# Performance work log

Measured on AMD Instinct MI355X. Metric: run time of the kernel, lower is better.

## Reference

```python
import jax, jax.numpy as jnp
import numpy as np

H, D = 16, 64            # heads_num, mouse_hidden_dim // heads_num
START_FRAME = 9728       # current_start (token units)
GLOBAL_END_PREV = 9728   # kv_cache['global_end_index'] before this call
LOCAL_END_PREV = 9728    # kv_cache['local_end_index'] before this call
SINK = 0                 # sink_tokens in source
WINDOW = 8192            # max_attention_size = local_attn_size (token units)


def _rope_interleaved(x, cos_h, sin_h):
    # non-neox (interleaved) rotary: x [B,S,H,D], cos_h/sin_h [S, D//2]
    x1 = x[..., 0::2]
    x2 = x[..., 1::2]
    c = cos_h[None, :, None, :]
    s = sin_h[None, :, None, :]
    o1 = x1 * c - x2 * s
    o2 = x2 * c + x1 * s
    return jnp.stack([o1, o2], axis=-1).reshape(x.shape)


def setup_inputs() -> dict:
    key = jax.random.key(0)
    ks = jax.random.split(key, 7)
    B, S, C = 1, 1024, 10240
    return {
        'q': jax.random.normal(ks[0], (B, S, H, D), jnp.float32),
        'k': jax.random.normal(ks[1], (B, S, H, D), jnp.float32),
        'v': jax.random.normal(ks[2], (B, S, H, D), jnp.float32),
        'cache_k': jax.random.normal(ks[3], (B, C, H, D), jnp.float32),
        'cache_v': jax.random.normal(ks[4], (B, C, H, D), jnp.float32),
        'freqs_cos': jax.random.uniform(ks[5], (START_FRAME + S, D), jnp.float32, -1.0, 1.0),
        'freqs_sin': jax.random.uniform(ks[6], (START_FRAME + S, D), jnp.float32, -1.0, 1.0),
    }


def reference(q, k, v, cache_k, cache_v, freqs_cos, freqs_sin):
    B, S, _, _ = q.shape
    # _apply_rotary_emb_qk: slice freqs at start_offset, take every-other col (cos_half)
    cos_h = freqs_cos[START_FRAME:START_FRAME + S, ::2]  # [S, D//2]
    sin_h = freqs_sin[START_FRAME:START_FRAME + S, ::2]
    q_r = _rope_interleaved(q, cos_h, sin_h)
    k_r = _rope_interleaved(k, cos_h, sin_h)

    # ring-buffer KV-cache update (all index math is static Python ints)
    current_end = START_FRAME + S
    cache_size = cache_k.shape[1]
    num_new = S
    if current_end > GLOBAL_END_PREV and num_new + LOCAL_END_PREV > cache_size:
        num_evicted = num_new + LOCAL_END_PREV - cache_size
        num_rolled = LOCAL_END_PREV - num_evicted - SINK
        rolled_k = jax.lax.dynamic_slice_in_dim(cache_k, SINK + num_evicted, num_rolled, axis=1)
        rolled_v = jax.lax.dynamic_slice_in_dim(cache_v, SINK + num_evicted, num_rolled, axis=1)
        cache_k = cache_k.at[:, SINK:SINK + num_rolled].set(rolled_k)
        cache_v = cache_v.at[:, SINK:SINK + num_rolled].set(rolled_v)
        local_end = LOCAL_END_PREV + current_end - GLOBAL_END_PREV - num_evicted
    else:
        local_end = LOCAL_END_PREV + current_end - GLOBAL_END_PREV
    local_start = local_end - num_new
    cache_k = cache_k.at[:, local_start:local_end].set(k_r)
    cache_v = cache_v.at[:, local_start:local_end].set(v)

    # windowed (last local_attn_size tokens) non-causal attention
    cache_start = max(0, local_end - WINDOW)
    wk = cache_k[:, cache_start:local_end]  # [B, W, H, D]
    wv = cache_v[:, cache_start:local_end]
    scale = 1.0 / np.float32(np.sqrt(D))
    scores = jnp.einsum('bqhd,bkhd->bhqk', q_r, wk) * scale
    probs = jax.nn.softmax(scores, axis=-1)
    out = jnp.einsum('bhqk,bkhd->bqhd', probs, wv)
    return out.reshape(B, S, H * D)
```

## Files before the change

kernel.cpp:

```cpp
#include <hip/hip_runtime.h>

#define HH 16
#define DD 64
#define SQ 1024
#define LW 8192
#define OLDK 7168
#define CACHE_BASE 2560
#define SFRAME 9728
#define KSPLIT 8
#define KPER (LW / KSPLIT)
#define NSTEP (KPER / 64)

#define KB_OFF 0u
#define VT_OFF 16777216u
#define QB_OFF 33554432u
#define OP_OFF 35651584u
#define LP_OFF 69206016u

typedef __bf16 bf16x8 __attribute__((ext_vector_type(8)));
typedef float floatx16 __attribute__((ext_vector_type(16)));
typedef float floatx2 __attribute__((ext_vector_type(2)));
typedef unsigned uintx2 __attribute__((ext_vector_type(2)));
typedef unsigned uintx4 __attribute__((ext_vector_type(4)));

__device__ __forceinline__ unsigned short f2bf(float f) {
  unsigned u = __builtin_bit_cast(unsigned, f);
  u += 0x7fffu + ((u >> 16) & 1u);
  return (unsigned short)(u >> 16);
}

__device__ __forceinline__ float fast_exp2(float x) {
#if __has_builtin(__builtin_amdgcn_exp2f)
  return __builtin_amdgcn_exp2f(x);
#else
  return __builtin_exp2f(x);
#endif
}

__device__ __forceinline__ unsigned pack_bf2(float a, float b) {
#if __has_builtin(__builtin_amdgcn_cvt_pk_bf16_f32)
  typedef __bf16 bf16x2_t __attribute__((ext_vector_type(2)));
  bf16x2_t r = __builtin_amdgcn_cvt_pk_bf16_f32(a, b);
  return __builtin_bit_cast(unsigned, r);
#else
  unsigned ua = __builtin_bit_cast(unsigned, a) + 0x8000u;
  unsigned ub = __builtin_bit_cast(unsigned, b) + 0x8000u;
  return __builtin_amdgcn_perm(ub, ua, 0x07060302);
#endif
}

__device__ __forceinline__ void async16(void* lds, const void* g) {
  __builtin_amdgcn_global_load_lds((__attribute__((address_space(1))) void*)(g),
                                   (__attribute__((address_space(3))) void*)(lds),
                                   16, 0, 0);
}

__global__ __launch_bounds__(256) void prepass(
    const float* __restrict__ qin, const float* __restrict__ kin,
    const float* __restrict__ vin, const float* __restrict__ ck,
    const float* __restrict__ cv, const float* __restrict__ fc,
    const float* __restrict__ fs, unsigned short* __restrict__ Kb,
    unsigned short* __restrict__ Vt, unsigned short* __restrict__ Qb) {
  __shared__ unsigned short tl[128 * 66];
  int b = blockIdx.x, t = threadIdx.x;
  if (b < 1024) {
    int h = b >> 6, kk0 = (b & 63) * 128;
    int c = t & 15;
#pragma unroll
    for (int it = 0; it < 8; it++) {
      int kk = it * 16 + (t >> 4);
      int gk = kk0 + kk;
      const float* src = (gk < OLDK)
                             ? cv + (CACHE_BASE + gk) * (HH * DD) + h * DD + 4 * c
                             : vin + (gk - OLDK) * (HH * DD) + h * DD + 4 * c;
      float4 vv = *(const float4*)src;
      ushort2 p0, p1;
      p0.x = f2bf(vv.x); p0.y = f2bf(vv.y);
      p1.x = f2bf(vv.z); p1.y = f2bf(vv.w);
      *(ushort2*)(tl + kk * 66 + 4 * c) = p0;
      *(ushort2*)(tl + kk * 66 + 4 * c + 2) = p1;
    }
    __syncthreads();
    int kq = t & 15;
#pragma unroll
    for (int jt = 0; jt < 4; jt++) {
      int d = jt * 16 + (t >> 4);
      ushort4 lo, hi;
      unsigned short tmp[8];
#pragma unroll
      for (int j = 0; j < 8; j++) {
        int kk = 8 * kq + j;
        tmp[j] = tl[kk * 66 + d];
      }
      lo.x = tmp[0]; lo.y = tmp[1]; lo.z = tmp[2]; lo.w = tmp[3];
      hi.x = tmp[4]; hi.y = tmp[5]; hi.z = tmp[6]; hi.w = tmp[7];
      unsigned short* dst = Vt + (h * DD + d) * LW + kk0 + 8 * kq;
      *(ushort4*)(dst) = lo;
      *(ushort4*)(dst + 4) = hi;
    }
  } else if (b < 8192) {
    int b1 = b - 1024;
    int h = b1 / 448, g = b1 % 448;
    int kk = g * 16 + (t >> 4);
    int lane = t & 15;
    float4 val = *(const float4*)(ck + (CACHE_BASE + kk) * (HH * DD) + h * DD + lane * 4);
    ushort4 o;
    o.x = f2bf(val.x); o.y = f2bf(val.y); o.z = f2bf(val.z); o.w = f2bf(val.w);
    *(ushort4*)(Kb + (h * LW + kk) * DD + lane * 4) = o;
  } else if (b < 10240) {
    int b2 = b - 8192;
    int rh = b2 * 8 + (t >> 5);
    int s = rh >> 4, h = rh & 15, i = t & 31;
    float2 x = *(const float2*)(kin + s * (HH * DD) + h * DD + 2 * i);
    float c = fc[(SFRAME + s) * DD + 2 * i];
    float sn = fs[(SFRAME + s) * DD + 2 * i];
    ushort2 o;
    o.x = f2bf(x.x * c - x.y * sn);
    o.y = f2bf(x.y * c + x.x * sn);
    *(ushort2*)(Kb + (h * LW + OLDK + s) * DD + 2 * i) = o;
  } else {
    int b3 = b - 10240;
    int rh = b3 * 8 + (t >> 5);
    int s = rh >> 4, h = rh & 15, i = t & 31;
    const float SC = 0.18033688011112042f;
    float2 x = *(const float2*)(qin + s * (HH * DD) + h * DD + 2 * i);
    float c = fc[(SFRAME + s) * DD + 2 * i];
    float sn = fs[(SFRAME + s) * DD + 2 * i];
    ushort2 o;
    o.x = f2bf((x.x * c - x.y * sn) * SC);
    o.y = f2bf((x.y * c + x.x * sn) * SC);
    *(ushort2*)(Qb + (h * SQ + s) * DD + 2 * i) = o;
  }
}

__global__ __launch_bounds__(256, 2) void attn(
    const unsigned short* __restrict__ Kb, const unsigned short* __restrict__ Vt,
    const unsigned short* __restrict__ Qb, unsigned short* __restrict__ Op,
    float* __restrict__ Lp) {
  __shared__ __align__(16) unsigned char sK[2][8192];
  __shared__ __align__(16) unsigned char sV[2][8192];

  int bid = blockIdx.x;
  int g = bid & 127, qb = bid >> 7;
  int h = g & 15, ks = g >> 4;
  int t = threadIdx.x;
  int w = t >> 6, lane = t & 63;
  int l31 = lane & 31, e = lane >> 5;
  int q0 = qb * 256 + w * 64;

  int baseA = (l31 & 7) ^ ((l31 >> 3) & 7);
  int baseB = (l31 & 7) ^ (((l31 >> 3) + 4) & 7);

  bf16x8 qf[2][4];
#pragma unroll
  for (int tq = 0; tq < 2; tq++) {
    const unsigned short* qptr = Qb + (h * SQ + q0 + 32 * tq + l31) * DD + 8 * e;
#pragma unroll
    for (int c = 0; c < 4; c++) qf[tq][c] = *(const bf16x8*)(qptr + 16 * c);
  }

  floatx16 o[2][2];
#pragma unroll
  for (int a = 0; a < 2; a++)
#pragma unroll
    for (int bb = 0; bb < 2; bb++)
#pragma unroll
      for (int i = 0; i < 16; i++) o[a][bb][i] = 0.f;
  float ls[2] = {0.f, 0.f};

  const floatx16 fz = {0.f};

  const unsigned short* KbH = Kb + h * (LW * DD);
  const unsigned short* VtH = Vt + h * (DD * LW);
  int kkBase = ks * KPER;

  int gi0 = w * 128 + lane;
  int gi1 = gi0 + 64;
  int rr0 = gi0 >> 3, rr1 = gi1 >> 3;
  int sw0 = (gi0 & 7) ^ (rr0 & 7) ^ ((rr0 >> 3) & 7);
  int sw1 = (gi1 & 7) ^ (rr1 & 7) ^ ((rr1 >> 3) & 7);
  const unsigned short* gK0 = KbH + (kkBase + rr0) * DD + sw0 * 8;
  const unsigned short* gK1 = KbH + (kkBase + rr1) * DD + sw1 * 8;
  const unsigned short* gV0 = VtH + rr0 * LW + kkBase + sw0 * 8;
  const unsigned short* gV1 = VtH + rr1 * LW + kkBase + sw1 * 8;
  int d0 = gi0 * 16, d1 = gi1 * 16;

  auto stage = [&](unsigned char* bK, unsigned char* bV) {
    async16(bK + d0, gK0);
    async16(bV + d0, gV0);
    async16(bK + d1, gK1);
    async16(bV + d1, gV1);
    gK0 += 64 * DD; gK1 += 64 * DD;
    gV0 += 64;      gV1 += 64;
  };

  auto softmax_half = [&](floatx16& sv, int tq, int tk, bf16x8 pf[2][4]) {
#pragma unroll
    for (int i = 0; i < 16; i++) sv[i] = fast_exp2(sv[i]);
    floatx2 t0, t1, t2, t3;
    t0[0] = sv[0];  t0[1] = sv[1];
    t1[0] = sv[2];  t1[1] = sv[3];
    t2[0] = sv[4];  t2[1] = sv[5];
    t3[0] = sv[6];  t3[1] = sv[7];
    floatx2 u0 = t0 + t1, u1 = t2 + t3;
    floatx2 t4, t5, t6, t7;
    t4[0] = sv[8];  t4[1] = sv[9];
    t5[0] = sv[10]; t5[1] = sv[11];
    t6[0] = sv[12]; t6[1] = sv[13];
    t7[0] = sv[14]; t7[1] = sv[15];
    floatx2 u2 = t4 + t5, u3 = t6 + t7;
    floatx2 v0 = u0 + u1, v1 = u2 + u3;
    floatx2 vs = v0 + v1;
    ls[tq] += vs[0] + vs[1];
#pragma unroll
    for (int kcp = 0; kcp < 2; kcp++) {
      unsigned u0p = pack_bf2(sv[8 * kcp + 0], sv[8 * kcp + 1]);
      unsigned u1p = pack_bf2(sv[8 * kcp + 2], sv[8 * kcp + 3]);
      unsigned u2p = pack_bf2(sv[8 * kcp + 4], sv[8 * kcp + 5]);
      unsigned u3p = pack_bf2(sv[8 * kcp + 6], sv[8 * kcp + 7]);
      uintx2 r0 = __builtin_amdgcn_permlane32_swap(u0p, u2p, false, false);
      uintx2 r1 = __builtin_amdgcn_permlane32_swap(u1p, u3p, false, false);
      uintx4 f;
      f[0] = r0[0]; f[1] = r1[0]; f[2] = r0[1]; f[3] = r1[1];
      pf[tq][2 * tk + kcp] = __builtin_bit_cast(bf16x8, f);
    }
  };

  auto step = [&](const unsigned char* cK, const unsigned char* cV,
                  bool doStage, unsigned char* nK, unsigned char* nV) {
    bf16x8 pf[2][4];

    floatx16 sA0, sA1;
    {
      int p0 = e ^ baseA;
      bf16x8 ka0 = *(const bf16x8*)(cK + (l31 * 8 + p0) * 16);
      sA0 = __builtin_amdgcn_mfma_f32_32x32x16_bf16(ka0, qf[0][0], fz, 0, 0, 0);
      sA1 = __builtin_amdgcn_mfma_f32_32x32x16_bf16(ka0, qf[1][0], fz, 0, 0, 0);
#pragma unroll
      for (int c = 1; c < 4; c++) {
        int p = (2 * c + e) ^ baseA;
        bf16x8 ka = *(const bf16x8*)(cK + (l31 * 8 + p) * 16);
        sA0 = __builtin_amdgcn_mfma_f32_32x32x16_bf16(ka, qf[0][c], sA0, 0, 0, 0);
        sA1 = __builtin_amdgcn_mfma_f32_32x32x16_bf16(ka, qf[1][c], sA1, 0, 0, 0);
      }
    }

    if (doStage) stage(nK, nV);

    floatx16 sB0, sB1;
    {
      int p0 = e ^ baseB;
      bf16x8 kb0 = *(const bf16x8*)(cK + ((l31 + 32) * 8 + p0) * 16);
      sB0 = __builtin_amdgcn_mfma_f32_32x32x16_bf16(kb0, qf[0][0], fz, 0, 0, 0);
      sB1 = __builtin_amdgcn_mfma_f32_32x32x16_bf16(kb0, qf[1][0], fz, 0, 0, 0);
#pragma unroll
      for (int c = 1; c < 4; c++) {
        int p = (2 * c + e) ^ baseB;
        bf16x8 kb = *(const bf16x8*)(cK + ((l31 + 32) * 8 + p) * 16);
        sB0 = __builtin_amdgcn_mfma_f32_32x32x16_bf16(kb, qf[0][c], sB0, 0, 0, 0);
        sB1 = __builtin_amdgcn_mfma_f32_32x32x16_bf16(kb, qf[1][c], sB1, 0, 0, 0);
      }
    }

    softmax_half(sA0, 0, 0, pf);
    softmax_half(sA1, 1, 0, pf);

#pragma unroll
    for (int kc = 0; kc < 2; kc++) {
      int pA = (2 * kc + e) ^ baseA;
      int pB = (2 * kc + e) ^ baseB;
      bf16x8 va = *(const bf16x8*)(cV + (l31 * 8 + pA) * 16);
      bf16x8 vb = *(const bf16x8*)(cV + ((l31 + 32) * 8 + pB) * 16);
      o[0][0] = __builtin_amdgcn_mfma_f32_32x32x16_bf16(va, pf[0][kc], o[0][0], 0, 0, 0);
      o[0][1] = __builtin_amdgcn_mfma_f32_32x32x16_bf16(vb, pf[0][kc], o[0][1], 0, 0, 0);
      o[1][0] = __builtin_amdgcn_mfma_f32_32x32x16_bf16(va, pf[1][kc], o[1][0], 0, 0, 0);
      o[1][1] = __builtin_amdgcn_mfma_f32_32x32x16_bf16(vb, pf[1][kc], o[1][1], 0, 0, 0);
    }

    softmax_half(sB0, 0, 1, pf);
    softmax_half(sB1, 1, 1, pf);

#pragma unroll
    for (int kc = 2; kc < 4; kc++) {
      int pA = (2 * kc + e) ^ baseA;
      int pB = (2 * kc + e) ^ baseB;
      bf16x8 va = *(const bf16x8*)(cV + (l31 * 8 + pA) * 16);
      bf16x8 vb = *(const bf16x8*)(cV + ((l31 + 32) * 8 + pB) * 16);
      o[0][0] = __builtin_amdgcn_mfma_f32_32x32x16_bf16(va, pf[0][kc], o[0][0], 0, 0, 0);
      o[0][1] = __builtin_amdgcn_mfma_f32_32x32x16_bf16(vb, pf[0][kc], o[0][1], 0, 0, 0);
      o[1][0] = __builtin_amdgcn_mfma_f32_32x32x16_bf16(va, pf[1][kc], o[1][0], 0, 0, 0);
      o[1][1] = __builtin_amdgcn_mfma_f32_32x32x16_bf16(vb, pf[1][kc], o[1][1], 0, 0, 0);
    }
  };

  stage(sK[0], sV[0]);

  for (int st = 0; st < NSTEP; st += 2) {
    __syncthreads();
    step(sK[0], sV[0], true, sK[1], sV[1]);
    __syncthreads();
    step(sK[1], sV[1], st + 2 < NSTEP, sK[0], sV[0]);
  }

#pragma unroll
  for (int tq = 0; tq < 2; tq++) {
    float l = ls[tq];
    l += __shfl_xor(l, 32, 64);
    int qrow = q0 + 32 * tq + l31;
    unsigned short* op = Op + (((ks * 16 + h) * SQ) + qrow) * DD;
#pragma unroll
    for (int t4 = 0; t4 < 4; t4++) {
      uint2 a, b;
      a.x = pack_bf2(o[tq][0][4 * t4 + 0], o[tq][0][4 * t4 + 1]);
      a.y = pack_bf2(o[tq][0][4 * t4 + 2], o[tq][0][4 * t4 + 3]);
      b.x = pack_bf2(o[tq][1][4 * t4 + 0], o[tq][1][4 * t4 + 1]);
      b.y = pack_bf2(o[tq][1][4 * t4 + 2], o[tq][1][4 * t4 + 3]);
      *(uint2*)(op + 8 * t4 + 4 * e) = a;
      *(uint2*)(op + 32 + 8 * t4 + 4 * e) = b;
    }
    if (e == 0) Lp[(ks * 16 + h) * SQ + qrow] = l;
  }
}

__global__ __launch_bounds__(256) void combine(const unsigned short* __restrict__ Op,
                                               const float* __restrict__ Lp,
                                               float* __restrict__ out) {
  int idx = blockIdx.x * 256 + threadIdx.x;
  int d4 = idx & 15, q = (idx >> 4) & 1023, h = idx >> 14;
  float num[4] = {0.f, 0.f, 0.f, 0.f};
  float den = 0.f;
#pragma unroll
  for (int s = 0; s < KSPLIT; s++) {
    int row = (s * 16 + h) * SQ + q;
    uint2 pkv = *(const uint2*)(Op + row * DD + 4 * d4);
    num[0] += __builtin_bit_cast(float, pkv.x << 16);
    num[1] += __builtin_bit_cast(float, pkv.x & 0xffff0000u);
    num[2] += __builtin_bit_cast(float, pkv.y << 16);
    num[3] += __builtin_bit_cast(float, pkv.y & 0xffff0000u);
    den += Lp[row];
  }
  float r = 1.0f / den;
  float4 ov;
  ov.x = num[0] * r; ov.y = num[1] * r; ov.z = num[2] * r; ov.w = num[3] * r;
  *(float4*)(out + q * (HH * DD) + h * DD + 4 * d4) = ov;
}

extern "C" void kernel_launch(void* const* d_in, const int* in_sizes, int n_in,
                              void* d_out, int out_size, void* d_ws, size_t ws_size,
                              hipStream_t stream) {
  const float* q  = (const float*)d_in[0];
  const float* k  = (const float*)d_in[1];
  const float* v  = (const float*)d_in[2];
  const float* ck = (const float*)d_in[3];
  const float* cv = (const float*)d_in[4];
  const float* fc = (const float*)d_in[5];
  const float* fs = (const float*)d_in[6];
  float* out = (float*)d_out;
  char* ws = (char*)d_ws;

  unsigned short* Kb = (unsigned short*)(ws + KB_OFF);
  unsigned short* Vt = (unsigned short*)(ws + VT_OFF);
  unsigned short* Qb = (unsigned short*)(ws + QB_OFF);
  unsigned short* Op = (unsigned short*)(ws + OP_OFF);
  float* Lp = (float*)(ws + LP_OFF);

  prepass<<<12288, 256, 0, stream>>>(q, k, v, ck, cv, fc, fs, Kb, Vt, Qb);
  attn<<<512, 256, 0, stream>>>(Kb, Vt, Qb, Op, Lp);
  combine<<<1024, 256, 0, stream>>>(Op, Lp, out);
}
```

Baseline: 174.4 us.

## Software-pipeline PV MFMAs of previous tile with QK of current tile

Splits the per-tile step into separate QK, softmax, V-load and PV phases and restructures the main loop as a software pipeline. Each iteration first runs the PV MFMAs of the previous tile, using V fragments already held in registers, then the QK MFMAs and softmax of the current tile. The aim is to let the exp/pack softmax work overlap with matrix-core work and to hide LDS read latency for V. The cost is more live registers (V fragments and all four score tiles), which may lower occupancy or cause spills, and the loop is no longer unrolled by two.

Result: no change. 174.7 us (+0.2%).

```diff
diff --git a/kernel.cpp b/kernel.cpp
--- a/kernel.cpp
+++ b/kernel.cpp
@@ -194,7 +194,11 @@
     gV0 += 64;      gV1 += 64;
   };
 
-  auto softmax_half = [&](floatx16& sv, int tq, int tk, bf16x8 pf[2][4]) {
+  bf16x8 pf[2][4];
+  bf16x8 vr[8];
+  floatx16 sA0, sA1, sB0, sB1;
+
+  auto softmax_half = [&](floatx16& sv, int tq, int tk) {
 #pragma unroll
     for (int i = 0; i < 16; i++) sv[i] = fast_exp2(sv[i]);
     floatx2 t0, t1, t2, t3;
@@ -226,11 +230,7 @@
     }
   };
 
-  auto step = [&](const unsigned char* cK, const unsigned char* cV,
-                  bool doStage, unsigned char* nK, unsigned char* nV) {
-    bf16x8 pf[2][4];
-
-    floatx16 sA0, sA1;
+  auto qk = [&](const unsigned char* cK) {
     {
       int p0 = e ^ baseA;
       bf16x8 ka0 = *(const bf16x8*)(cK + (l31 * 8 + p0) * 16);
@@ -244,10 +244,6 @@
         sA1 = __builtin_amdgcn_mfma_f32_32x32x16_bf16(ka, qf[1][c], sA1, 0, 0, 0);
       }
     }
-
-    if (doStage) stage(nK, nV);
-
-    floatx16 sB0, sB1;
     {
       int p0 = e ^ baseB;
       bf16x8 kb0 = *(const bf16x8*)(cK + ((l31 + 32) * 8 + p0) * 16);
@@ -261,46 +257,56 @@
         sB1 = __builtin_amdgcn_mfma_f32_32x32x16_bf16(kb, qf[1][c], sB1, 0, 0, 0);
       }
     }
-
-    softmax_half(sA0, 0, 0, pf);
-    softmax_half(sA1, 1, 0, pf);
-
-#pragma unroll
-    for (int kc = 0; kc < 2; kc++) {
+  };
+
+  auto sm_all = [&]() {
+    softmax_half(sA0, 0, 0);
+    softmax_half(sA1, 1, 0);
+    softmax_half(sB0, 0, 1);
+    softmax_half(sB1, 1, 1);
+  };
+
+  auto vload = [&](const unsigned char* cV) {
+#pragma unroll
+    for (int kc = 0; kc < 4; kc++) {
       int pA = (2 * kc + e) ^ baseA;
       int pB = (2 * kc + e) ^ baseB;
-      bf16x8 va = *(const bf16x8*)(cV + (l31 * 8 + pA) * 16);
-      bf16x8 vb = *(const bf16x8*)(cV + ((l31 + 32) * 8 + pB) * 16);
-      o[0][0] = __builtin_amdgcn_mfma_f32_32x32x16_bf16(va, pf[0][kc], o[0][0], 0, 0, 0);
-      o[0][1] = __builtin_amdgcn_mfma_f32_32x32x16_bf16(vb, pf[0][kc], o[0][1], 0, 0, 0);
-      o[1][0] = __builtin_amdgcn_mfma_f32_32x32x16_bf16(va, pf[1][kc], o[1][0], 0, 0, 0);
-      o[1][1] = __builtin_amdgcn_mfma_f32_32x32x16_bf16(vb, pf[1][kc], o[1][1], 0, 0, 0);
-    }
-
-    softmax_half(sB0, 0, 1, pf);
-    softmax_half(sB1, 1, 1, pf);
-
-#pragma unroll
-    for (int kc = 2; kc < 4; kc++) {
-      int pA = (2 * kc + e) ^ baseA;
-      int pB = (2 * kc + e) ^ baseB;
-      bf16x8 va = *(const bf16x8*)(cV + (l31 * 8 + pA) * 16);
-      bf16x8 vb = *(const bf16x8*)(cV + ((l31 + 32) * 8 + pB) * 16);
-      o[0][0] = __builtin_amdgcn_mfma_f32_32x32x16_bf16(va, pf[0][kc], o[0][0], 0, 0, 0);
-      o[0][1] = __builtin_amdgcn_mfma_f32_32x32x16_bf16(vb, pf[0][kc], o[0][1], 0, 0, 0);
-      o[1][0] = __builtin_amdgcn_mfma_f32_32x32x16_bf16(va, pf[1][kc], o[1][0], 0, 0, 0);
-      o[1][1] = __builtin_amdgcn_mfma_f32_32x32x16_bf16(vb, pf[1][kc], o[1][1], 0, 0, 0);
+      vr[2 * kc]     = *(const bf16x8*)(cV + (l31 * 8 + pA) * 16);
+      vr[2 * kc + 1] = *(const bf16x8*)(cV + ((l31 + 32) * 8 + pB) * 16);
+    }
+  };
+
+  auto pv = [&]() {
+#pragma unroll
+    for (int kc = 0; kc < 4; kc++) {
+      o[0][0] = __builtin_amdgcn_mfma_f32_32x32x16_bf16(vr[2 * kc], pf[0][kc], o[0][0], 0, 0, 0);
+      o[0][1] = __builtin_amdgcn_mfma_f32_32x32x16_bf16(vr[2 * kc + 1], pf[0][kc], o[0][1], 0, 0, 0);
+      o[1][0] = __builtin_amdgcn_mfma_f32_32x32x16_bf16(vr[2 * kc], pf[1][kc], o[1][0], 0, 0, 0);
+      o[1][1] = __builtin_amdgcn_mfma_f32_32x32x16_bf16(vr[2 * kc + 1], pf[1][kc], o[1][1], 0, 0, 0);
     }
   };
 
   stage(sK[0], sV[0]);
-
-  for (int st = 0; st < NSTEP; st += 2) {
+  __syncthreads();
+  qk(sK[0]);
+  stage(sK[1], sV[1]);
+  sm_all();
+  vload(sV[0]);
+
+  for (int st = 1; st < NSTEP; st++) {
     __syncthreads();
-    step(sK[0], sV[0], true, sK[1], sV[1]);
-    __syncthreads();
-    step(sK[1], sV[1], st + 2 < NSTEP, sK[0], sV[0]);
-  }
+    const unsigned char* cK = (st & 1) ? sK[1] : sK[0];
+    const unsigned char* cV = (st & 1) ? sV[1] : sV[0];
+    unsigned char* nK = (st & 1) ? sK[0] : sK[1];
+    unsigned char* nV = (st & 1) ? sV[0] : sV[1];
+
+    pv();
+    qk(cK);
+    if (st + 1 < NSTEP) stage(nK, nV);
+    sm_all();
+    vload(cV);
+  }
+  pv();
 
 #pragma unroll
   for (int tq = 0; tq < 2; tq++) {
```
